# Optimization experiments

Measured on AMD Instinct MI355X. Metric: run time of the kernel, lower is better.

## Reference

```python
import jax, jax.numpy as jnp
import numpy as np

N_NODES = 100000
N_EDGES = 1600000
DIM = 128


def setup_inputs() -> dict:
    key = jax.random.key(0)
    ks = jax.random.split(key, 8)
    s = 1.0 / np.sqrt(DIM)
    return {
        "x": jax.random.normal(ks[0], (N_NODES, DIM), dtype=jnp.float32),
        "edge_index": jax.random.randint(ks[1], (2, N_EDGES), 0, N_NODES, dtype=jnp.int64),
        "W1_l": jax.random.normal(ks[2], (DIM, DIM), dtype=jnp.float32) * s,
        "b1": jnp.zeros((DIM,), dtype=jnp.float32),
        "W1_r": jax.random.normal(ks[3], (DIM, DIM), dtype=jnp.float32) * s,
        "W2_l": jax.random.normal(ks[4], (DIM, DIM), dtype=jnp.float32) * s,
        "b2": jnp.zeros((DIM,), dtype=jnp.float32),
        "W2_r": jax.random.normal(ks[5], (DIM, DIM), dtype=jnp.float32) * s,
    }


def _sage_conv(h, src, dst, n, W_l, b, W_r):
    # mean aggregation of source-node features onto target nodes
    agg = jax.ops.segment_sum(h[src], dst, num_segments=n)          # [N, D]
    deg = jax.ops.segment_sum(jnp.ones_like(src, dtype=h.dtype), dst, num_segments=n)
    agg = agg / jnp.maximum(deg, 1.0)[:, None]
    # PyG SAGEConv: lin_l(aggr) + bias + lin_r(x)  (root weight, no bias on lin_r)
    return agg @ W_l + b + h @ W_r


def reference(x, edge_index, W1_l, b1, W1_r, W2_l, b2, W2_r):
    src, dst = edge_index[0], edge_index[1]
    n = x.shape[0]
    h = jax.nn.relu(_sage_conv(x, src, dst, n, W1_l, b1, W1_r))
    return _sage_conv(h, src, dst, n, W2_l, b2, W2_r)
```

## Files before the change

### kernel.cpp

```cpp
#include <hip/hip_runtime.h>

typedef unsigned short ushort_t;
typedef unsigned int uint_t;

typedef short bf16x8 __attribute__((ext_vector_type(8)));
typedef float f32x4 __attribute__((ext_vector_type(4)));

#define DIM 128
#define BSHIFT 8
#define BNODES 256
#define DBINS 64

__device__ __forceinline__ float bf2f(ushort_t u) {
    uint_t x = ((uint_t)u) << 16;
    float f;
    __builtin_memcpy(&f, &x, 4);
    return f;
}

__device__ __forceinline__ ushort_t f2bf(float f) {
    uint_t x;
    __builtin_memcpy(&x, &f, 4);
    uint_t r = (x + 0x7fffu + ((x >> 16) & 1u)) >> 16;
    return (ushort_t)r;
}


__global__ __launch_bounds__(256) void k_prep_bhist(
        const float* __restrict__ x, ushort_t* __restrict__ xb, int n4,
        const float* __restrict__ W0, const float* __restrict__ W1,
        const float* __restrict__ W2, const float* __restrict__ W3,
        ushort_t* __restrict__ T0, ushort_t* __restrict__ T1,
        ushort_t* __restrict__ T2, ushort_t* __restrict__ T3,
        const int* __restrict__ dst, int E, int NB, int* __restrict__ bucketCount,
        int prepBlocks) {
    if ((int)blockIdx.x >= prepBlocks) {
        __shared__ int hist[512];
        int blk = blockIdx.x - prepBlocks;
        int t = threadIdx.x;
        for (int b = t; b < NB; b += 256) hist[b] = 0;
        __syncthreads();
        int per = (E + 255) / 256;
        int beg = blk * per, end = min(beg + per, E);
        for (int i = beg + t; i < end; i += 256)
            atomicAdd(&hist[dst[i] >> BSHIFT], 1);
        __syncthreads();
        for (int b = t; b < NB; b += 256) {
            int v = hist[b];
            if (v) atomicAdd(&bucketCount[b], v);
        }
        return;
    }
    int i = blockIdx.x * 256 + threadIdx.x;
    if (i < n4) {
        float4 f = ((const float4*)x)[i];
        ushort4 u;
        u.x = f2bf(f.x); u.y = f2bf(f.y); u.z = f2bf(f.z); u.w = f2bf(f.w);
        ((ushort4*)xb)[i] = u;
    } else {
        int j = i - n4;
        if (j < 4 * DIM * DIM) {
            int w = j >> 14; j &= 16383;
            int n = j >> 7, k = j & 127;
            const float* W = (w == 0) ? W0 : (w == 1) ? W1 : (w == 2) ? W2 : W3;
            ushort_t* T = (w == 0) ? T0 : (w == 1) ? T1 : (w == 2) ? T2 : T3;
            T[j] = f2bf(W[k * DIM + n]);
        }
    }
}


__global__ __launch_bounds__(512) void k_bscan(const int* __restrict__ bucketCount, int NB, int E,
                                               int* __restrict__ bucketBase,
                                               int* __restrict__ bucketCursor,
                                               int* __restrict__ row_ptr, int N) {
    __shared__ int lds[512];
    int t = threadIdx.x;
    int v = (t < NB) ? bucketCount[t] : 0;
    lds[t] = v;
    __syncthreads();
    for (int off = 1; off < 512; off <<= 1) {
        int u = (t >= off) ? lds[t - off] : 0;
        __syncthreads();
        lds[t] += u;
        __syncthreads();
    }
    if (t < NB) {
        int b = lds[t] - v;
        bucketBase[t] = b;
        bucketCursor[t] = b;
    }
    if (t == 0) row_ptr[N] = E;
}

__global__ __launch_bounds__(256) void k_bucketize(const int* __restrict__ src,
                                                   const int* __restrict__ dst, int E, int NB,
                                                   int* __restrict__ bucketCursor,
                                                   uint_t* __restrict__ bebuf) {
    __shared__ int hist[512];
    __shared__ int base[512];
    int t = threadIdx.x;
    for (int b = t; b < NB; b += 256) hist[b] = 0;
    __syncthreads();
    int per = (E + gridDim.x - 1) / gridDim.x;
    int beg = blockIdx.x * per, end = min(beg + per, E);
    for (int i = beg + t; i < end; i += 256)
        atomicAdd(&hist[dst[i] >> BSHIFT], 1);
    __syncthreads();
    for (int b = t; b < NB; b += 256) {
        int v = hist[b];
        base[b] = v ? atomicAdd(&bucketCursor[b], v) : 0;
        hist[b] = 0;
    }
    __syncthreads();
    for (int i = beg + t; i < end; i += 256) {
        int d = dst[i], s = src[i];
        int b = d >> BSHIFT;
        int off = atomicAdd(&hist[b], 1);
        bebuf[base[b] + off] = ((uint_t)(d & (BNODES - 1)) << 24) | (uint_t)s;
    }
}

__global__ __launch_bounds__(256) void k_bcsr(const uint_t* __restrict__ bebuf,
                                              const int* __restrict__ bucketBase,
                                              const int* __restrict__ bucketCount, int N,
                                              int* __restrict__ row_ptr, int* __restrict__ csr,
                                              int* __restrict__ dhist) {
    __shared__ int hist[BNODES];
    __shared__ int cur[BNODES];
    __shared__ int dh[DBINS];
    int t = threadIdx.x;
    int b = blockIdx.x;
    int ebase = bucketBase[b], cnt = bucketCount[b];
    int nodeBase = b << BSHIFT;
    hist[t] = 0;
    if (t < DBINS) dh[t] = 0;
    __syncthreads();
    for (int i = t; i < cnt; i += 256)
        atomicAdd(&hist[bebuf[ebase + i] >> 24], 1);
    __syncthreads();
    int v = hist[t];
    int node = nodeBase + t;
    if (node < N) atomicAdd(&dh[min(v, DBINS - 1)], 1);
    for (int off = 1; off < 256; off <<= 1) {
        int u = (t >= off) ? hist[t - off] : 0;
        __syncthreads();
        hist[t] += u;
        __syncthreads();
    }
    int excl = hist[t] - v;
    if (node < N) row_ptr[node] = ebase + excl;
    cur[t] = excl;
    __syncthreads();
    for (int i = t; i < cnt; i += 256) {
        uint_t e = bebuf[ebase + i];
        int dl = (int)(e >> 24);
        int pos = atomicAdd(&cur[dl], 1);
        csr[ebase + pos] = (int)(e & 0xFFFFFFu);
    }
    __syncthreads();
    if (t < DBINS) {
        int c = dh[t];
        if (c) atomicAdd(&dhist[t], c);
    }
}


__global__ void k_dscan(const int* __restrict__ dhist, int* __restrict__ dcur) {
    __shared__ int l[DBINS];
    int t = threadIdx.x;
    int v = dhist[t];
    l[t] = v;
    __syncthreads();
    for (int off = 1; off < DBINS; off <<= 1) {
        int u = (t >= off) ? l[t - off] : 0;
        __syncthreads();
        l[t] += u;
        __syncthreads();
    }
    dcur[t] = l[t] - v;
}

__global__ __launch_bounds__(256) void k_dperm(const int* __restrict__ rp, int N,
                                               int* __restrict__ dcur, int* __restrict__ perm) {
    __shared__ int h[DBINS];
    __shared__ int base[DBINS];
    int t = threadIdx.x;
    if (t < DBINS) h[t] = 0;
    __syncthreads();
    int i = blockIdx.x * 256 + t;
    int b = -1;
    if (i < N) {
        int d = rp[i + 1] - rp[i];
        b = min(d, DBINS - 1);
        atomicAdd(&h[b], 1);
    }
    __syncthreads();
    if (t < DBINS) {
        int v = h[t];
        base[t] = v ? atomicAdd(&dcur[t], v) : 0;
        h[t] = 0;
    }
    __syncthreads();
    if (i < N) {
        int off = atomicAdd(&h[b], 1);
        perm[base[b] + off] = i;
    }
}


__device__ __forceinline__ void acc8(float* a, uint4 p) {
    union { uint_t u; float f; } c;
    c.u = p.x << 16;         a[0] += c.f;
    c.u = p.x & 0xffff0000u; a[1] += c.f;
    c.u = p.y << 16;         a[2] += c.f;
    c.u = p.y & 0xffff0000u; a[3] += c.f;
    c.u = p.z << 16;         a[4] += c.f;
    c.u = p.z & 0xffff0000u; a[5] += c.f;
    c.u = p.w << 16;         a[6] += c.f;
    c.u = p.w & 0xffff0000u; a[7] += c.f;
}

__global__ __launch_bounds__(256) void k_agg(const ushort_t* __restrict__ X,
                                             const int* __restrict__ row_ptr,
                                             const int* __restrict__ csr,
                                             const int* __restrict__ perm,
                                             ushort_t* __restrict__ out, int n) {
    int g = (int)((blockIdx.x * (unsigned)blockDim.x + threadIdx.x) >> 4);
    if (g >= n) return;
    int node = perm[g];
    int sl = threadIdx.x & 15;
    int beg = row_ptr[node], end = row_ptr[node + 1];
    float a[8] = {0.f, 0.f, 0.f, 0.f, 0.f, 0.f, 0.f, 0.f};

    int e = beg;
    for (; e + 4 <= end; e += 4) {
        int s0 = csr[e + 0], s1 = csr[e + 1], s2 = csr[e + 2], s3 = csr[e + 3];
        uint4 p0 = *(const uint4*)(X + (size_t)s0 * DIM + sl * 8);
        uint4 p1 = *(const uint4*)(X + (size_t)s1 * DIM + sl * 8);
        uint4 p2 = *(const uint4*)(X + (size_t)s2 * DIM + sl * 8);
        uint4 p3 = *(const uint4*)(X + (size_t)s3 * DIM + sl * 8);
        acc8(a, p0); acc8(a, p1); acc8(a, p2); acc8(a, p3);
    }
    for (; e < end; e++) {
        int s = csr[e];
        uint4 p = *(const uint4*)(X + (size_t)s * DIM + sl * 8);
        acc8(a, p);
    }

    int cnt = end - beg;
    float sc = (cnt > 0) ? 1.f / (float)cnt : 0.f;
    uint4 o;
    o.x = (uint_t)f2bf(a[0] * sc) | ((uint_t)f2bf(a[1] * sc) << 16);
    o.y = (uint_t)f2bf(a[2] * sc) | ((uint_t)f2bf(a[3] * sc) << 16);
    o.z = (uint_t)f2bf(a[4] * sc) | ((uint_t)f2bf(a[5] * sc) << 16);
    o.w = (uint_t)f2bf(a[6] * sc) | ((uint_t)f2bf(a[7] * sc) << 16);
    *(uint4*)(out + (size_t)node * DIM + sl * 8) = o;
}


template <bool RELU, bool OUT_BF16>
struct GemmBody {
    const ushort_t* A1;
    const ushort_t* A2;
    const ushort_t* sW;
    void* Out;
    int M;
    int w, col, quad;
    float bv[8];

    __device__ __forceinline__ void loadA(bf16x8 (&a)[2][8], int tile) const {
#pragma unroll
        for (int tt = 0; tt < 2; tt++) {
            int arow = tile * 128 + w * 32 + tt * 16 + col;
            const ushort_t* a1p = A1 + (size_t)arow * DIM + quad * 8;
            const ushort_t* a2p = A2 + (size_t)arow * DIM + quad * 8;
#pragma unroll
            for (int ks = 0; ks < 4; ks++) a[tt][ks] = *(const bf16x8*)(a1p + ks * 32);
#pragma unroll
            for (int ks = 0; ks < 4; ks++) a[tt][4 + ks] = *(const bf16x8*)(a2p + ks * 32);
        }
    }

    __device__ __forceinline__ void compute(const bf16x8 (&a)[2][8], int tile) const {
        f32x4 acc[2][8];
#pragma unroll
        for (int tt = 0; tt < 2; tt++)
#pragma unroll
            for (int nt = 0; nt < 8; nt++) acc[tt][nt] = (f32x4){0.f, 0.f, 0.f, 0.f};

        const ushort_t* sWl = sW;
        const ushort_t* sWr = sW + 128 * 128;
        __builtin_amdgcn_s_setprio(1);
#pragma unroll
        for (int nt = 0; nt < 8; nt++) {
            int row = nt * 16 + col;
            const ushort_t* bl = sWl + (size_t)row * 128;
            const ushort_t* br = sWr + (size_t)row * 128;
#pragma unroll
            for (int ks = 0; ks < 4; ks++) {
                bf16x8 b = *(const bf16x8*)(bl + (((ks * 4 + quad) ^ col) * 8));
                acc[0][nt] = __builtin_amdgcn_mfma_f32_16x16x32_bf16(a[0][ks], b, acc[0][nt], 0, 0, 0);
                acc[1][nt] = __builtin_amdgcn_mfma_f32_16x16x32_bf16(a[1][ks], b, acc[1][nt], 0, 0, 0);
            }
#pragma unroll
            for (int ks = 0; ks < 4; ks++) {
                bf16x8 b = *(const bf16x8*)(br + (((ks * 4 + quad) ^ col) * 8));
                acc[0][nt] = __builtin_amdgcn_mfma_f32_16x16x32_bf16(a[0][4 + ks], b, acc[0][nt], 0, 0, 0);
                acc[1][nt] = __builtin_amdgcn_mfma_f32_16x16x32_bf16(a[1][4 + ks], b, acc[1][nt], 0, 0, 0);
            }
        }
        __builtin_amdgcn_s_setprio(0);

#pragma unroll
        for (int tt = 0; tt < 2; tt++)
#pragma unroll
            for (int nt = 0; nt < 8; nt++) {
                int c = nt * 16 + col;
#pragma unroll
                for (int r = 0; r < 4; r++) {
                    int m = tile * 128 + w * 32 + tt * 16 + quad * 4 + r;
                    if (m < M) {
                        float v = acc[tt][nt][r] + bv[nt];
                        if (RELU) v = v > 0.f ? v : 0.f;
                        if (OUT_BF16)
                            ((ushort_t*)Out)[(size_t)m * DIM + c] = f2bf(v);
                        else
                            ((float*)Out)[(size_t)m * DIM + c] = v;
                    }
                }
            }
    }
};

template <bool RELU, bool OUT_BF16>
__global__ __launch_bounds__(256, 2) void k_gemm(const ushort_t* __restrict__ A1,
                                                 const ushort_t* __restrict__ A2,
                                                 const ushort_t* __restrict__ WTl,
                                                 const ushort_t* __restrict__ WTr,
                                                 const float* __restrict__ bias,
                                                 void* __restrict__ Out, int ntiles, int M) {
    __shared__ ushort_t sW[2 * 128 * 128];
    int t = threadIdx.x;

    GemmBody<RELU, OUT_BF16> gb;
    gb.A1 = A1; gb.A2 = A2; gb.sW = sW; gb.Out = Out; gb.M = M;
    gb.w = t >> 6;
    int lane = t & 63;
    gb.col = lane & 15;
    gb.quad = lane >> 4;
#pragma unroll
    for (int nt = 0; nt < 8; nt++) gb.bv[nt] = bias[nt * 16 + gb.col];

    int tile = blockIdx.x;
    bf16x8 aA[2][8], aB[2][8];
    gb.loadA(aA, tile);

    {
        int tab = t >> 7, row = t & 127;
        const ushort_t* g = (tab ? WTr : WTl) + (size_t)row * 128;
        ushort_t* d = sW + (size_t)t * 128;
        int sw = row & 15;
#pragma unroll
        for (int c = 0; c < 16; c++) {
            uint4 v = *(const uint4*)(g + c * 8);
            *(uint4*)(d + ((c ^ sw) * 8)) = v;
        }
    }
    __syncthreads();

    int step = gridDim.x;
    while (true) {
        int t2 = tile + step;
        if (t2 < ntiles) gb.loadA(aB, t2);
        gb.compute(aA, tile);
        tile = t2;
        if (tile >= ntiles) break;

        int t3 = tile + step;
        if (t3 < ntiles) gb.loadA(aA, t3);
        gb.compute(aB, tile);
        tile = t3;
        if (tile >= ntiles) break;
    }
}


extern "C" void kernel_launch(void* const* d_in, const int* in_sizes, int n_in,
                              void* d_out, int out_size, void* d_ws, size_t ws_size,
                              hipStream_t stream) {
    const int N = in_sizes[0] / DIM;
    const int E = in_sizes[1] / 2;
    const int NB = (N + BNODES - 1) >> BSHIFT;

    const float* x   = (const float*)d_in[0];
    const int*   ei  = (const int*)d_in[1];
    const int*   src = ei;
    const int*   dst = ei + E;
    const float* W1l = (const float*)d_in[2];
    const float* b1  = (const float*)d_in[3];
    const float* W1r = (const float*)d_in[4];
    const float* W2l = (const float*)d_in[5];
    const float* b2  = (const float*)d_in[6];
    const float* W2r = (const float*)d_in[7];
    float* out = (float*)d_out;

    char* ws = (char*)d_ws;
    size_t off = 0;
    auto alloc = [&](size_t bytes) -> char* {
        char* p = ws + off;
        off = (off + bytes + 255) & ~(size_t)255;
        return p;
    };

    int*      bucketCount  = (int*)alloc((size_t)NB * 4);
    int*      dhist        = (int*)alloc((size_t)DBINS * 4);
    int*      dcur         = (int*)alloc((size_t)DBINS * 4);
    int*      bucketBase   = (int*)alloc((size_t)NB * 4);
    int*      bucketCursor = (int*)alloc((size_t)NB * 4);
    int*      row_ptr      = (int*)alloc((size_t)(N + 1) * 4);
    int*      csr          = (int*)alloc((size_t)E * 4);
    uint_t*   bebuf        = (uint_t*)alloc((size_t)E * 4);
    size_t    fpad         = (size_t)128 * DIM * 2;
    ushort_t* xb           = (ushort_t*)alloc((size_t)N * DIM * 2 + fpad);
    ushort_t* hb           = (ushort_t*)alloc((size_t)N * DIM * 2 + fpad);
    ushort_t* aggb         = (ushort_t*)alloc((size_t)N * DIM * 2 + fpad);
    ushort_t* wt1l         = (ushort_t*)alloc((size_t)DIM * DIM * 2);
    ushort_t* wt1r         = (ushort_t*)alloc((size_t)DIM * DIM * 2);
    ushort_t* wt2l         = (ushort_t*)alloc((size_t)DIM * DIM * 2);
    ushort_t* wt2r         = (ushort_t*)alloc((size_t)DIM * DIM * 2);
    int*      perm         = (int*)bebuf;

    hipMemsetAsync(bucketCount, 0, (size_t)((char*)dhist - (char*)bucketCount) + DBINS * 4, stream);

    {
        int n4 = N * DIM / 4;
        int total = n4 + 4 * DIM * DIM;
        int prepBlocks = (total + 255) / 256;
        k_prep_bhist<<<dim3(prepBlocks + 256), dim3(256), 0, stream>>>(
            x, xb, n4, W1l, W1r, W2l, W2r, wt1l, wt1r, wt2l, wt2r,
            dst, E, NB, bucketCount, prepBlocks);
    }
    k_bscan<<<dim3(1), dim3(512), 0, stream>>>(bucketCount, NB, E, bucketBase, bucketCursor, row_ptr, N);
    k_bucketize<<<dim3(256), dim3(256), 0, stream>>>(src, dst, E, NB, bucketCursor, bebuf);
    k_bcsr<<<dim3(NB), dim3(256), 0, stream>>>(bebuf, bucketBase, bucketCount, N, row_ptr, csr, dhist);

    const int nblk = (N + 255) / 256;
    k_dscan<<<dim3(1), dim3(DBINS), 0, stream>>>(dhist, dcur);
    k_dperm<<<dim3(nblk), dim3(256), 0, stream>>>(row_ptr, N, dcur, perm);

    const int ntiles = (N + 127) / 128;
    dim3 gemm_grid((unsigned)min(ntiles, 512)), gemm_blk(256);
    dim3 agg_grid((N + 15) / 16), agg_blk(256);

    k_agg<<<agg_grid, agg_blk, 0, stream>>>(xb, row_ptr, csr, perm, aggb, N);
    k_gemm<true, true><<<gemm_grid, gemm_blk, 0, stream>>>(aggb, xb, wt1l, wt1r, b1, hb, ntiles, N);
    k_agg<<<agg_grid, agg_blk, 0, stream>>>(hb, row_ptr, csr, perm, aggb, N);
    k_gemm<false, false><<<gemm_grid, gemm_blk, 0, stream>>>(aggb, hb, wt2l, wt2r, b2, out, ntiles, N);

    (void)n_in; (void)out_size; (void)ws_size;
}
```

Measured before the change: 354.6 us.

## Fuse mean aggregation with GEMM per 16-node tile and fold scans into consumers

Each 16-node block now computes the mean aggregation, stages the aggregated row and the node's own features in swizzled LDS, and runs MFMA against weights pre-packed into per-lane fragment layout in global memory. This removes the separate aggregation buffer and its write and re-read, and drops two GEMM launches. The bucket and degree prefix scans are redundantly recomputed inside k_bucketize and k_dperm to eliminate two single-block launches. In exchange, weight fragments are read from global or L2 by every block instead of being staged once per persistent block, and output stores are scattered per node via perm.

```diff
diff --git a/kernel.cpp b/kernel.cpp
--- a/kernel.cpp
+++ b/kernel.cpp
@@ -10,13 +10,6 @@
 #define BSHIFT 8
 #define BNODES 256
 #define DBINS 64
-
-__device__ __forceinline__ float bf2f(ushort_t u) {
-    uint_t x = ((uint_t)u) << 16;
-    float f;
-    __builtin_memcpy(&f, &x, 4);
-    return f;
-}
 
 __device__ __forceinline__ ushort_t f2bf(float f) {
     uint_t x;
@@ -28,10 +21,9 @@
 
 __global__ __launch_bounds__(256) void k_prep_bhist(
         const float* __restrict__ x, ushort_t* __restrict__ xb, int n4,
-        const float* __restrict__ W0, const float* __restrict__ W1,
-        const float* __restrict__ W2, const float* __restrict__ W3,
-        ushort_t* __restrict__ T0, ushort_t* __restrict__ T1,
-        ushort_t* __restrict__ T2, ushort_t* __restrict__ T3,
+        const float* __restrict__ W1l, const float* __restrict__ W1r,
+        const float* __restrict__ W2l, const float* __restrict__ W2r,
+        ushort_t* __restrict__ fragbuf,
         const int* __restrict__ dst, int E, int NB, int* __restrict__ bucketCount,
         int prepBlocks) {
     if ((int)blockIdx.x >= prepBlocks) {
@@ -59,65 +51,79 @@
         ((ushort4*)xb)[i] = u;
     } else {
         int j = i - n4;
-        if (j < 4 * DIM * DIM) {
-            int w = j >> 14; j &= 16383;
-            int n = j >> 7, k = j & 127;
-            const float* W = (w == 0) ? W0 : (w == 1) ? W1 : (w == 2) ? W2 : W3;
-            ushort_t* T = (w == 0) ? T0 : (w == 1) ? T1 : (w == 2) ? T2 : T3;
-            T[j] = f2bf(W[k * DIM + n]);
+        if (j < 2 * 64 * 64) {
+            int layer = j >> 12;
+            int rr = j & 4095;
+            int f = rr >> 6, l = rr & 63;
+            int nt = f >> 3, ks2 = f & 7;
+            int col = l & 15, quad = l >> 4;
+            int n = nt * 16 + col;
+            int kb = ks2 * 32 + quad * 8;
+            const float* Wl = layer ? W2l : W1l;
+            const float* Wr = layer ? W2r : W1r;
+            ushort_t* d = fragbuf + layer * 32768 + f * 512 + l * 8;
+#pragma unroll
+            for (int jj = 0; jj < 8; jj++) {
+                int k2 = kb + jj;
+                float v = (k2 < 128) ? Wl[k2 * DIM + n] : Wr[(k2 - 128) * DIM + n];
+                d[jj] = f2bf(v);
+            }
         }
     }
 }
 
-
-__global__ __launch_bounds__(512) void k_bscan(const int* __restrict__ bucketCount, int NB, int E,
-                                               int* __restrict__ bucketBase,
-                                               int* __restrict__ bucketCursor,
-                                               int* __restrict__ row_ptr, int N) {
-    __shared__ int lds[512];
-    int t = threadIdx.x;
-    int v = (t < NB) ? bucketCount[t] : 0;
-    lds[t] = v;
-    __syncthreads();
-    for (int off = 1; off < 512; off <<= 1) {
-        int u = (t >= off) ? lds[t - off] : 0;
-        __syncthreads();
-        lds[t] += u;
-        __syncthreads();
-    }
-    if (t < NB) {
-        int b = lds[t] - v;
-        bucketBase[t] = b;
-        bucketCursor[t] = b;
-    }
-    if (t == 0) row_ptr[N] = E;
-}
 
 __global__ __launch_bounds__(256) void k_bucketize(const int* __restrict__ src,
                                                    const int* __restrict__ dst, int E, int NB,
-                                                   int* __restrict__ bucketCursor,
+                                                   const int* __restrict__ bucketCount,
+                                                   int* __restrict__ bucketBase_out,
+                                                   int* __restrict__ row_ptr, int N,
+                                                   int* __restrict__ zcur,
                                                    uint_t* __restrict__ bebuf) {
+    __shared__ int bbase[512];
     __shared__ int hist[512];
-    __shared__ int base[512];
+    __shared__ int rbase[512];
     int t = threadIdx.x;
-    for (int b = t; b < NB; b += 256) hist[b] = 0;
+    int i0 = t, i1 = t + 256;
+    int v0 = (i0 < NB) ? bucketCount[i0] : 0;
+    int v1 = (i1 < NB) ? bucketCount[i1] : 0;
+    bbase[i0] = v0; bbase[i1] = v1;
+    __syncthreads();
+    for (int off = 1; off < 512; off <<= 1) {
+        int u0 = (i0 >= off) ? bbase[i0 - off] : 0;
+        int u1 = (i1 >= off) ? bbase[i1 - off] : 0;
+        __syncthreads();
+        bbase[i0] += u0; bbase[i1] += u1;
+        __syncthreads();
+    }
+    bbase[i0] -= v0;
+    bbase[i1] -= v1;
+    if (blockIdx.x == 0) {
+        if (i0 < NB) bucketBase_out[i0] = bbase[i0];
+        if (i1 < NB) bucketBase_out[i1] = bbase[i1];
+        if (t == 0) row_ptr[N] = E;
+    }
+    hist[i0] = 0; hist[i1] = 0;
     __syncthreads();
     int per = (E + gridDim.x - 1) / gridDim.x;
     int beg = blockIdx.x * per, end = min(beg + per, E);
     for (int i = beg + t; i < end; i += 256)
         atomicAdd(&hist[dst[i] >> BSHIFT], 1);
     __syncthreads();
-    for (int b = t; b < NB; b += 256) {
-        int v = hist[b];
-        base[b] = v ? atomicAdd(&bucketCursor[b], v) : 0;
-        hist[b] = 0;
+    {
+        int v = hist[i0];
+        rbase[i0] = v ? (bbase[i0] + atomicAdd(&zcur[i0], v)) : 0;
+        hist[i0] = 0;
+        v = hist[i1];
+        rbase[i1] = v ? (bbase[i1] + atomicAdd(&zcur[i1], v)) : 0;
+        hist[i1] = 0;
     }
     __syncthreads();
     for (int i = beg + t; i < end; i += 256) {
         int d = dst[i], s = src[i];
         int b = d >> BSHIFT;
         int off = atomicAdd(&hist[b], 1);
-        bebuf[base[b] + off] = ((uint_t)(d & (BNODES - 1)) << 24) | (uint_t)s;
+        bebuf[rbase[b] + off] = ((uint_t)(d & (BNODES - 1)) << 24) | (uint_t)s;
     }
 }
 
@@ -166,28 +172,23 @@
 }
 
 
-__global__ void k_dscan(const int* __restrict__ dhist, int* __restrict__ dcur) {
-    __shared__ int l[DBINS];
+__global__ __launch_bounds__(256) void k_dperm(const int* __restrict__ rp, int N,
+                                               const int* __restrict__ dhist,
+                                               int* __restrict__ zdcur, int* __restrict__ perm) {
+    __shared__ int eb[DBINS];
+    __shared__ int h[DBINS];
+    __shared__ int rb[DBINS];
     int t = threadIdx.x;
-    int v = dhist[t];
-    l[t] = v;
+    int v = (t < DBINS) ? dhist[t] : 0;
+    if (t < DBINS) { eb[t] = v; h[t] = 0; }
     __syncthreads();
     for (int off = 1; off < DBINS; off <<= 1) {
-        int u = (t >= off) ? l[t - off] : 0;
-        __syncthreads();
-        l[t] += u;
-        __syncthreads();
-    }
-    dcur[t] = l[t] - v;
-}
-
-__global__ __launch_bounds__(256) void k_dperm(const int* __restrict__ rp, int N,
-                                               int* __restrict__ dcur, int* __restrict__ perm) {
-    __shared__ int h[DBINS];
-    __shared__ int base[DBINS];
-    int t = threadIdx.x;
-    if (t < DBINS) h[t] = 0;
-    __syncthreads();
+        int u = (t < DBINS && t >= off) ? eb[t - off] : 0;
+        __syncthreads();
+        if (t < DBINS) eb[t] += u;
+        __syncthreads();
+    }
+    if (t < DBINS) eb[t] -= v;
     int i = blockIdx.x * 256 + t;
     int b = -1;
     if (i < N) {
@@ -197,14 +198,14 @@
     }
     __syncthreads();
     if (t < DBINS) {
-        int v = h[t];
-        base[t] = v ? atomicAdd(&dcur[t], v) : 0;
+        int hv = h[t];
+        rb[t] = hv ? (eb[t] + atomicAdd(&zdcur[t], hv)) : 0;
         h[t] = 0;
     }
     __syncthreads();
     if (i < N) {
         int off = atomicAdd(&h[b], 1);
-        perm[base[b] + off] = i;
+        perm[rb[b] + off] = i;
     }
 }
 
@@ -221,18 +222,30 @@
     c.u = p.w & 0xffff0000u; a[7] += c.f;
 }
 
-__global__ __launch_bounds__(256) void k_agg(const ushort_t* __restrict__ X,
-                                             const int* __restrict__ row_ptr,
-                                             const int* __restrict__ csr,
-                                             const int* __restrict__ perm,
-                                             ushort_t* __restrict__ out, int n) {
-    int g = (int)((blockIdx.x * (unsigned)blockDim.x + threadIdx.x) >> 4);
-    if (g >= n) return;
-    int node = perm[g];
-    int sl = threadIdx.x & 15;
-    int beg = row_ptr[node], end = row_ptr[node + 1];
+template <bool RELU, bool OUT_BF16>
+__global__ __launch_bounds__(256) void k_fused(const ushort_t* __restrict__ X,
+                                               const int* __restrict__ row_ptr,
+                                               const int* __restrict__ csr,
+                                               const int* __restrict__ perm,
+                                               const ushort_t* __restrict__ fragbuf,
+                                               const float* __restrict__ bias,
+                                               void* __restrict__ Out, int N) {
+    __shared__ __align__(16) ushort_t tile[16 * 256];
+    __shared__ int nd[16];
+    int t = threadIdx.x;
+    int gl = t >> 4;
+    int sl = t & 15;
+    int gidx = blockIdx.x * 16 + gl;
+    bool act = (gidx < N);
+    int node = 0, beg = 0, end = 0;
+    if (act) {
+        node = perm[gidx];
+        beg = row_ptr[node];
+        end = row_ptr[node + 1];
+    }
+    if (sl == 0) nd[gl] = node;
+
     float a[8] = {0.f, 0.f, 0.f, 0.f, 0.f, 0.f, 0.f, 0.f};
-
     int e = beg;
     for (; e + 4 <= end; e += 4) {
         int s0 = csr[e + 0], s1 = csr[e + 1], s2 = csr[e + 2], s3 = csr[e + 3];
@@ -247,141 +260,64 @@
         uint4 p = *(const uint4*)(X + (size_t)s * DIM + sl * 8);
         acc8(a, p);
     }
-
     int cnt = end - beg;
-    float sc = (cnt > 0) ? 1.f / (float)cnt : 0.f;
+    float scl = (cnt > 0) ? 1.f / (float)cnt : 0.f;
+
+    int swz = gl & 7;
     uint4 o;
-    o.x = (uint_t)f2bf(a[0] * sc) | ((uint_t)f2bf(a[1] * sc) << 16);
-    o.y = (uint_t)f2bf(a[2] * sc) | ((uint_t)f2bf(a[3] * sc) << 16);
-    o.z = (uint_t)f2bf(a[4] * sc) | ((uint_t)f2bf(a[5] * sc) << 16);
-    o.w = (uint_t)f2bf(a[6] * sc) | ((uint_t)f2bf(a[7] * sc) << 16);
-    *(uint4*)(out + (size_t)node * DIM + sl * 8) = o;
-}
-
-
-template <bool RELU, bool OUT_BF16>
-struct GemmBody {
-    const ushort_t* A1;
-    const ushort_t* A2;
-    const ushort_t* sW;
-    void* Out;
-    int M;
-    int w, col, quad;
-    float bv[8];
-
-    __device__ __forceinline__ void loadA(bf16x8 (&a)[2][8], int tile) const {
-#pragma unroll
-        for (int tt = 0; tt < 2; tt++) {
-            int arow = tile * 128 + w * 32 + tt * 16 + col;
-            const ushort_t* a1p = A1 + (size_t)arow * DIM + quad * 8;
-            const ushort_t* a2p = A2 + (size_t)arow * DIM + quad * 8;
-#pragma unroll
-            for (int ks = 0; ks < 4; ks++) a[tt][ks] = *(const bf16x8*)(a1p + ks * 32);
-#pragma unroll
-            for (int ks = 0; ks < 4; ks++) a[tt][4 + ks] = *(const bf16x8*)(a2p + ks * 32);
-        }
-    }
-
-    __device__ __forceinline__ void compute(const bf16x8 (&a)[2][8], int tile) const {
-        f32x4 acc[2][8];
-#pragma unroll
-        for (int tt = 0; tt < 2; tt++)
-#pragma unroll
-            for (int nt = 0; nt < 8; nt++) acc[tt][nt] = (f32x4){0.f, 0.f, 0.f, 0.f};
-
-        const ushort_t* sWl = sW;
-        const ushort_t* sWr = sW + 128 * 128;
-        __builtin_amdgcn_s_setprio(1);
-#pragma unroll
-        for (int nt = 0; nt < 8; nt++) {
-            int row = nt * 16 + col;
-            const ushort_t* bl = sWl + (size_t)row * 128;
-            const ushort_t* br = sWr + (size_t)row * 128;
-#pragma unroll
-            for (int ks = 0; ks < 4; ks++) {
-                bf16x8 b = *(const bf16x8*)(bl + (((ks * 4 + quad) ^ col) * 8));
-                acc[0][nt] = __builtin_amdgcn_mfma_f32_16x16x32_bf16(a[0][ks], b, acc[0][nt], 0, 0, 0);
-                acc[1][nt] = __builtin_amdgcn_mfma_f32_16x16x32_bf16(a[1][ks], b, acc[1][nt], 0, 0, 0);
-            }
-#pragma unroll
-            for (int ks = 0; ks < 4; ks++) {
-                bf16x8 b = *(const bf16x8*)(br + (((ks * 4 + quad) ^ col) * 8));
-                acc[0][nt] = __builtin_amdgcn_mfma_f32_16x16x32_bf16(a[0][4 + ks], b, acc[0][nt], 0, 0, 0);
-                acc[1][nt] = __builtin_amdgcn_mfma_f32_16x16x32_bf16(a[1][4 + ks], b, acc[1][nt], 0, 0, 0);
+    o.x = (uint_t)f2bf(a[0] * scl) | ((uint_t)f2bf(a[1] * scl) << 16);
+    o.y = (uint_t)f2bf(a[2] * scl) | ((uint_t)f2bf(a[3] * scl) << 16);
+    o.z = (uint_t)f2bf(a[4] * scl) | ((uint_t)f2bf(a[5] * scl) << 16);
+    o.w = (uint_t)f2bf(a[6] * scl) | ((uint_t)f2bf(a[7] * scl) << 16);
+    *(uint4*)(tile + gl * 256 + ((sl ^ swz) * 8)) = o;
+    uint4 p;
+    if (act) p = *(const uint4*)(X + (size_t)node * DIM + sl * 8);
+    else     p = (uint4){0u, 0u, 0u, 0u};
+    *(uint4*)(tile + gl * 256 + (((16 + sl) ^ swz) * 8)) = p;
+    __syncthreads();
+
+    int lane = t & 63, w = t >> 6;
+    int m = lane & 15, quad = lane >> 4;
+    bf16x8 af[8];
+#pragma unroll
+    for (int ks2 = 0; ks2 < 8; ks2++) {
+        int c = (ks2 * 4 + quad) ^ (m & 7);
+        af[ks2] = *(const bf16x8*)(tile + m * 256 + c * 8);
+    }
+    f32x4 acc0 = (f32x4){0.f, 0.f, 0.f, 0.f};
+    f32x4 acc1 = (f32x4){0.f, 0.f, 0.f, 0.f};
+    const ushort_t* fb0 = fragbuf + (size_t)((w * 2 + 0) * 8) * 512 + lane * 8;
+    const ushort_t* fb1 = fragbuf + (size_t)((w * 2 + 1) * 8) * 512 + lane * 8;
+#pragma unroll
+    for (int ks2 = 0; ks2 < 8; ks2++) {
+        bf16x8 b0 = *(const bf16x8*)(fb0 + ks2 * 512);
+        acc0 = __builtin_amdgcn_mfma_f32_16x16x32_bf16(af[ks2], b0, acc0, 0, 0, 0);
+    }
+#pragma unroll
+    for (int ks2 = 0; ks2 < 8; ks2++) {
+        bf16x8 b1 = *(const bf16x8*)(fb1 + ks2 * 512);
+        acc1 = __builtin_amdgcn_mfma_f32_16x16x32_bf16(af[ks2], b1, acc1, 0, 0, 0);
+    }
+    int c0 = (w * 2 + 0) * 16 + m;
+    int c1 = (w * 2 + 1) * 16 + m;
+    float bv0 = bias[c0], bv1 = bias[c1];
+#pragma unroll
+    for (int r = 0; r < 4; r++) {
+        int mrow = quad * 4 + r;
+        int gI = blockIdx.x * 16 + mrow;
+        if (gI < N) {
+            int nodeW = nd[mrow];
+            float v0 = acc0[r] + bv0;
+            float v1 = acc1[r] + bv1;
+            if (RELU) { v0 = fmaxf(v0, 0.f); v1 = fmaxf(v1, 0.f); }
+            if (OUT_BF16) {
+                ((ushort_t*)Out)[(size_t)nodeW * DIM + c0] = f2bf(v0);
+                ((ushort_t*)Out)[(size_t)nodeW * DIM + c1] = f2bf(v1);
+            } else {
+                ((float*)Out)[(size_t)nodeW * DIM + c0] = v0;
+                ((float*)Out)[(size_t)nodeW * DIM + c1] = v1;
             }
         }
-        __builtin_amdgcn_s_setprio(0);
-
-#pragma unroll
-        for (int tt = 0; tt < 2; tt++)
-#pragma unroll
-            for (int nt = 0; nt < 8; nt++) {
-                int c = nt * 16 + col;
-#pragma unroll
-                for (int r = 0; r < 4; r++) {
-                    int m = tile * 128 + w * 32 + tt * 16 + quad * 4 + r;
-                    if (m < M) {
-                        float v = acc[tt][nt][r] + bv[nt];
-                        if (RELU) v = v > 0.f ? v : 0.f;
-                        if (OUT_BF16)
-                            ((ushort_t*)Out)[(size_t)m * DIM + c] = f2bf(v);
-                        else
-                            ((float*)Out)[(size_t)m * DIM + c] = v;
-                    }
-                }
-            }
-    }
-};
-
-template <bool RELU, bool OUT_BF16>
-__global__ __launch_bounds__(256, 2) void k_gemm(const ushort_t* __restrict__ A1,
-                                                 const ushort_t* __restrict__ A2,
-                                                 const ushort_t* __restrict__ WTl,
-                                                 const ushort_t* __restrict__ WTr,
-                                                 const float* __restrict__ bias,
-                                                 void* __restrict__ Out, int ntiles, int M) {
-    __shared__ ushort_t sW[2 * 128 * 128];
-    int t = threadIdx.x;
-
-    GemmBody<RELU, OUT_BF16> gb;
-    gb.A1 = A1; gb.A2 = A2; gb.sW = sW; gb.Out = Out; gb.M = M;
-    gb.w = t >> 6;
-    int lane = t & 63;
-    gb.col = lane & 15;
-    gb.quad = lane >> 4;
-#pragma unroll
-    for (int nt = 0; nt < 8; nt++) gb.bv[nt] = bias[nt * 16 + gb.col];
-
-    int tile = blockIdx.x;
-    bf16x8 aA[2][8], aB[2][8];
-    gb.loadA(aA, tile);
-
-    {
-        int tab = t >> 7, row = t & 127;
-        const ushort_t* g = (tab ? WTr : WTl) + (size_t)row * 128;
-        ushort_t* d = sW + (size_t)t * 128;
-        int sw = row & 15;
-#pragma unroll
-        for (int c = 0; c < 16; c++) {
-            uint4 v = *(const uint4*)(g + c * 8);
-            *(uint4*)(d + ((c ^ sw) * 8)) = v;
-        }
-    }
-    __syncthreads();
-
-    int step = gridDim.x;
-    while (true) {
-        int t2 = tile + step;
-        if (t2 < ntiles) gb.loadA(aB, t2);
-        gb.compute(aA, tile);
-        tile = t2;
-        if (tile >= ntiles) break;
-
-        int t3 = tile + step;
-        if (t3 < ntiles) gb.loadA(aA, t3);
-        gb.compute(aB, tile);
-        tile = t3;
-        if (tile >= ntiles) break;
     }
 }
 
@@ -415,48 +351,40 @@
 
     int*      bucketCount  = (int*)alloc((size_t)NB * 4);
     int*      dhist        = (int*)alloc((size_t)DBINS * 4);
-    int*      dcur         = (int*)alloc((size_t)DBINS * 4);
+    int*      zcur         = (int*)alloc((size_t)NB * 4);
+    int*      zdcur        = (int*)alloc((size_t)DBINS * 4);
+    size_t    zspan        = (size_t)((char*)zdcur + DBINS * 4 - (char*)bucketCount);
     int*      bucketBase   = (int*)alloc((size_t)NB * 4);
-    int*      bucketCursor = (int*)alloc((size_t)NB * 4);
     int*      row_ptr      = (int*)alloc((size_t)(N + 1) * 4);
     int*      csr          = (int*)alloc((size_t)E * 4);
     uint_t*   bebuf        = (uint_t*)alloc((size_t)E * 4);
-    size_t    fpad         = (size_t)128 * DIM * 2;
-    ushort_t* xb           = (ushort_t*)alloc((size_t)N * DIM * 2 + fpad);
-    ushort_t* hb           = (ushort_t*)alloc((size_t)N * DIM * 2 + fpad);
-    ushort_t* aggb         = (ushort_t*)alloc((size_t)N * DIM * 2 + fpad);
-    ushort_t* wt1l         = (ushort_t*)alloc((size_t)DIM * DIM * 2);
-    ushort_t* wt1r         = (ushort_t*)alloc((size_t)DIM * DIM * 2);
-    ushort_t* wt2l         = (ushort_t*)alloc((size_t)DIM * DIM * 2);
-    ushort_t* wt2r         = (ushort_t*)alloc((size_t)DIM * DIM * 2);
+    ushort_t* xb           = (ushort_t*)alloc((size_t)N * DIM * 2);
+    ushort_t* hb           = (ushort_t*)alloc((size_t)N * DIM * 2);
+    ushort_t* fragbuf      = (ushort_t*)alloc((size_t)2 * 32768 * 2);
     int*      perm         = (int*)bebuf;
 
-    hipMemsetAsync(bucketCount, 0, (size_t)((char*)dhist - (char*)bucketCount) + DBINS * 4, stream);
+    hipMemsetAsync(bucketCount, 0, zspan, stream);
 
     {
         int n4 = N * DIM / 4;
-        int total = n4 + 4 * DIM * DIM;
+        int total = n4 + 2 * 64 * 64;
         int prepBlocks = (total + 255) / 256;
         k_prep_bhist<<<dim3(prepBlocks + 256), dim3(256), 0, stream>>>(
-            x, xb, n4, W1l, W1r, W2l, W2r, wt1l, wt1r, wt2l, wt2r,
+            x, xb, n4, W1l, W1r, W2l, W2r, fragbuf,
             dst, E, NB, bucketCount, prepBlocks);
     }
-    k_bscan<<<dim3(1), dim3(512), 0, stream>>>(bucketCount, NB, E, bucketBase, bucketCursor, row_ptr, N);
-    k_bucketize<<<dim3(256), dim3(256), 0, stream>>>(src, dst, E, NB, bucketCursor, bebuf);
-    k_bcsr<<<dim3(NB), dim3(256), 0, stream>>>(bebuf, bucketBase, bucketCount, N, row_ptr, csr, dhist);
-
+    k_bucketize<<<dim3(256), dim3(256), 0, stream>>>(src, dst, E, NB, bucketCount,
+                                                     bucketBase, row_ptr, N, zcur, bebuf);
+    k_bcsr<<<dim3(NB), dim3(256), 0, stream>>>(bebuf, bucketBase, bucketCount, N,
+                                               row_ptr, csr, dhist);
     const int nblk = (N + 255) / 256;
-    k_dscan<<<dim3(1), dim3(DBINS), 0, stream>>>(dhist, dcur);
-    k_dperm<<<dim3(nblk), dim3(256), 0, stream>>>(row_ptr, N, dcur, perm);
-
-    const int ntiles = (N + 127) / 128;
-    dim3 gemm_grid((unsigned)min(ntiles, 512)), gemm_blk(256);
-    dim3 agg_grid((N + 15) / 16), agg_blk(256);
-
-    k_agg<<<agg_grid, agg_blk, 0, stream>>>(xb, row_ptr, csr, perm, aggb, N);
-    k_gemm<true, true><<<gemm_grid, gemm_blk, 0, stream>>>(aggb, xb, wt1l, wt1r, b1, hb, ntiles, N);
-    k_agg<<<agg_grid, agg_blk, 0, stream>>>(hb, row_ptr, csr, perm, aggb, N);
-    k_gemm<false, false><<<gemm_grid, gemm_blk, 0, stream>>>(aggb, hb, wt2l, wt2r, b2, out, ntiles, N);
+    k_dperm<<<dim3(nblk), dim3(256), 0, stream>>>(row_ptr, N, dhist, zdcur, perm);
+
+    const int ntiles = (N + 15) / 16;
+    k_fused<true, true><<<dim3(ntiles), dim3(256), 0, stream>>>(
+        xb, row_ptr, csr, perm, fragbuf, b1, hb, N);
+    k_fused<false, false><<<dim3(ntiles), dim3(256), 0, stream>>>(
+        hb, row_ptr, csr, perm, fragbuf + 32768, b2, out, N);
 
     (void)n_in; (void)out_size; (void)ws_size;
 }
```

After: 319.7 us. -9.9%, faster.
